# Kernel tuning notes

Hardware: AMD Instinct MI355X
Metric: run time of the kernel (lower is better)

Reference implementation:

```python
import jax, jax.numpy as jnp
import numpy as np

EPS = 1e-12
CHAMFER_W, NORM_W, EDGE_W = 1.0, 0.1, 0.5


def setup_inputs() -> dict:
    key = jax.random.key(0)
    ks = jax.random.split(key, 6)
    B, V, F, N = 8, 6890, 13776, 4096
    return {
        "predicted_vertices": jax.random.normal(ks[0], (B, V, 3), jnp.float32),
        "predicted_faces": jax.random.randint(ks[1], (F, 3), 0, V),
        "gt_vertices": jax.random.normal(ks[2], (B, V, 3), jnp.float32),
        "gt_faces": jax.random.randint(ks[3], (F, 3), 0, V),
        "rand_pred": jax.random.uniform(ks[4], (B, N, 3), jnp.float32),
        "rand_gt": jax.random.uniform(ks[5], (B, N, 3), jnp.float32),
    }


def _sample_points(vertices, faces, rnd):
    """Area-weighted surface sampling. vertices [B,V,3], faces [F,3], rnd [B,N,3].
    Returns (points [B,N,3], normals [B,N,3])."""
    tri = vertices[:, faces]                       # [B,F,3,3]
    v0, v1, v2 = tri[:, :, 0], tri[:, :, 1], tri[:, :, 2]
    cross = jnp.cross(v1 - v0, v2 - v0)            # [B,F,3]
    cn = jnp.linalg.norm(cross, axis=-1)           # [B,F]
    area = 0.5 * cn
    normals = cross / (cn[..., None] + EPS)
    cdf = jnp.cumsum(area, axis=1)
    cdf = cdf / (cdf[:, -1:] + EPS)
    u, r1, r2 = rnd[..., 0], rnd[..., 1], rnd[..., 2]
    idx = jax.vmap(jnp.searchsorted)(cdf, u)       # [B,N] inverse-CDF face pick
    idx = jnp.clip(idx, 0, faces.shape[0] - 1)
    g = lambda x: jnp.take_along_axis(x, idx[..., None], axis=1)
    p0, p1, p2 = g(v0), g(v1), g(v2)
    su = jnp.sqrt(r1)[..., None]                   # sqrt trick -> uniform barycentric
    w0 = 1.0 - su
    w1 = su * (1.0 - r2[..., None])
    w2 = su * r2[..., None]
    return w0 * p0 + w1 * p1 + w2 * p2, g(normals)


def reference(predicted_vertices, predicted_faces, gt_vertices, gt_faces, rand_pred, rand_gt):
    # NOTE: faithful to the source, which samples BOTH clouds from the predicted
    # mesh (copy-paste bug): gt cloud = second independent sample of pred mesh.
    pc, pn = _sample_points(predicted_vertices, predicted_faces, rand_pred)
    gc, gn = _sample_points(predicted_vertices, predicted_faces, rand_gt)

    # squared-distance chamfer: [B,N,N]
    d = (jnp.sum(pc * pc, -1)[:, :, None]
         + jnp.sum(gc * gc, -1)[:, None, :]
         - 2.0 * jnp.einsum('bnd,bmd->bnm', pc, gc))
    dist1 = jnp.min(d, axis=2)
    dist2 = jnp.min(d, axis=1)
    chamfer_loss = jnp.mean(dist1) + jnp.mean(dist2)

    # normal loss: cosine mismatch with nearest-neighbor normals
    nn = jnp.argmin(d, axis=2)                     # [B,N]
    gn_nn = jnp.take_along_axis(gn, nn[..., None], axis=1)
    norm_loss = jnp.mean(1.0 - jnp.abs(jnp.sum(pn * gn_nn, axis=-1)))

    # edge loss: mean squared edge length over the 3 edges of every face
    pv, pf = predicted_vertices, predicted_faces
    e01 = pv[:, pf[:, 0]] - pv[:, pf[:, 1]]
    e12 = pv[:, pf[:, 1]] - pv[:, pf[:, 2]]
    e20 = pv[:, pf[:, 2]] - pv[:, pf[:, 0]]
    edge_loss = (jnp.mean(jnp.sum(e01 * e01, -1))
                 + jnp.mean(jnp.sum(e12 * e12, -1))
                 + jnp.mean(jnp.sum(e20 * e20, -1))) / 3.0

    return CHAMFER_W * chamfer_loss + NORM_W * norm_loss + EDGE_W * edge_loss
```

## Files before the change

kernel.cpp:

```cpp
#include <hip/hip_runtime.h>

#define EPSF 1e-12f
#define FLTMAX 3.402823466e+38f

constexpr int B = 8, V = 6890, F = 13776, N = 4096;
constexpr int BF = B * F;
constexpr int BN = B * N;
constexpr int CHUNK = 512;
constexpr int NCHUNK = (F + CHUNK - 1) / CHUNK;

__device__ __forceinline__ unsigned enc_f(float f) {
  unsigned b = __float_as_uint(f);
  return (b & 0x80000000u) ? ~b : (b | 0x80000000u);
}
__device__ __forceinline__ float dec_f(unsigned u) {
  return (u & 0x80000000u) ? __uint_as_float(u & 0x7FFFFFFFu) : __uint_as_float(~u);
}

__device__ __forceinline__ float block_sum_256(float v, float* s4) {
  #pragma unroll
  for (int off = 32; off > 0; off >>= 1) v += __shfl_down(v, off, 64);
  __syncthreads();
  if ((threadIdx.x & 63) == 0) s4[threadIdx.x >> 6] = v;
  __syncthreads();
  return s4[0] + s4[1] + s4[2] + s4[3];
}

__global__ void init_kernel(unsigned long long* __restrict__ best1,
                            unsigned* __restrict__ best2, float* __restrict__ acc) {
  int i = blockIdx.x * 256 + threadIdx.x;
  best1[i] = ~0ull;
  best2[i] = ~0u;
  if (i < 4) acc[i] = 0.f;
}

__global__ void face_kernel(const float* __restrict__ pv, const int* __restrict__ pf,
                            float* __restrict__ area, float* __restrict__ nrm,
                            float* __restrict__ acc) {
  __shared__ float s4[4];
  int idx = blockIdx.x * 256 + threadIdx.x;
  float es = 0.f;
  if (idx < BF) {
    int b = idx / F, f = idx - b * F;
    int i0 = pf[f * 3 + 0], i1 = pf[f * 3 + 1], i2 = pf[f * 3 + 2];
    const float* vb = pv + (size_t)b * V * 3;
    float x0 = vb[i0 * 3 + 0], y0 = vb[i0 * 3 + 1], z0 = vb[i0 * 3 + 2];
    float x1 = vb[i1 * 3 + 0], y1 = vb[i1 * 3 + 1], z1 = vb[i1 * 3 + 2];
    float x2 = vb[i2 * 3 + 0], y2 = vb[i2 * 3 + 1], z2 = vb[i2 * 3 + 2];
    float ax = x1 - x0, ay = y1 - y0, az = z1 - z0;
    float bx = x2 - x0, by = y2 - y0, bz = z2 - z0;
    float cx = ay * bz - az * by;
    float cy = az * bx - ax * bz;
    float cz = ax * by - ay * bx;
    float cn = sqrtf(cx * cx + cy * cy + cz * cz);
    area[idx] = 0.5f * cn;
    float inv = 1.f / (cn + EPSF);
    nrm[(size_t)idx * 3 + 0] = cx * inv;
    nrm[(size_t)idx * 3 + 1] = cy * inv;
    nrm[(size_t)idx * 3 + 2] = cz * inv;
    float ex = x0 - x1, ey = y0 - y1, ez = z0 - z1;
    es = ex * ex + ey * ey + ez * ez;
    ex = x1 - x2; ey = y1 - y2; ez = z1 - z2;
    es += ex * ex + ey * ey + ez * ez;
    es += bx * bx + by * by + bz * bz;
  }
  float tot = block_sum_256(es, s4);
  if (threadIdx.x == 0) atomicAdd(&acc[3], tot);
}

__global__ void scan_chunks(float* __restrict__ cdf, float* __restrict__ csum) {
  int b = blockIdx.x / NCHUNK, ck = blockIdx.x % NCHUNK;
  float* c = cdf + (size_t)b * F;
  int lane = threadIdx.x & 63, wid = threadIdx.x >> 6;
  int i0 = ck * CHUNK + 2 * threadIdx.x, i1 = i0 + 1;
  float a0 = (i0 < F) ? c[i0] : 0.f;
  float a1 = (i1 < F) ? c[i1] : 0.f;
  float ts = a0 + a1;
  float x = ts;
  #pragma unroll
  for (int off = 1; off < 64; off <<= 1) {
    float y = __shfl_up(x, off, 64);
    if (lane >= off) x += y;
  }
  __shared__ float wsum[4];
  if (lane == 63) wsum[wid] = x;
  __syncthreads();
  float woff = 0.f;
  for (int w = 0; w < wid; ++w) woff += wsum[w];
  float excl = woff + x - ts;
  if (i0 < F) c[i0] = excl + a0;
  if (i1 < F) c[i1] = excl + ts;
  if (threadIdx.x == 255) csum[b * NCHUNK + ck] = woff + x;
}

__global__ void scan_sums(float* __restrict__ csum, float* __restrict__ totals) {
  int b = threadIdx.x;
  if (b < B) {
    float s = 0.f;
    for (int k = 0; k < NCHUNK; ++k) { s += csum[b * NCHUNK + k]; csum[b * NCHUNK + k] = s; }
    totals[b] = s;
  }
}

__global__ void sample_kernel(const float* __restrict__ pv, const int* __restrict__ pf,
                              const float* __restrict__ cdf, const float* __restrict__ csum,
                              const float* __restrict__ totals, const float* __restrict__ nrm,
                              const float* __restrict__ rp, const float* __restrict__ rg,
                              float* __restrict__ pc, float* __restrict__ pn,
                              float* __restrict__ gc, float* __restrict__ gn) {
  int idx = blockIdx.x * 256 + threadIdx.x;
  if (idx >= 2 * BN) return;
  int set = (idx >= BN) ? 1 : 0;
  int i = idx - set * BN;
  int b = i / N;
  const float* r = (set ? rg : rp) + (size_t)i * 3;
  float u = r[0], r1 = r[1], r2 = r[2];
  float target = u * (totals[b] + EPSF);
  const float* cs = csum + b * NCHUNK;
  int lo = 0, hi = NCHUNK;
  while (lo < hi) { int mid = (lo + hi) >> 1; if (cs[mid] < target) lo = mid + 1; else hi = mid; }
  int k = lo < NCHUNK ? lo : NCHUNK - 1;
  float off = (k > 0) ? cs[k - 1] : 0.f;
  float t2 = target - off;
  const float* c = cdf + (size_t)b * F;
  int base = k * CHUNK;
  int lo2 = 0, hi2 = CHUNK;
  while (lo2 < hi2) {
    int mid = (lo2 + hi2) >> 1;
    int gi = base + mid;
    float v = (gi < F) ? c[gi] : FLTMAX;
    if (v < t2) lo2 = mid + 1; else hi2 = mid;
  }
  int f = base + lo2;
  if (f > F - 1) f = F - 1;
  int i0 = pf[f * 3 + 0], i1 = pf[f * 3 + 1], i2 = pf[f * 3 + 2];
  const float* vb = pv + (size_t)b * V * 3;
  float su = sqrtf(r1);
  float w0 = 1.f - su, w1 = su * (1.f - r2), w2 = su * r2;
  float px = w0 * vb[i0 * 3 + 0] + w1 * vb[i1 * 3 + 0] + w2 * vb[i2 * 3 + 0];
  float py = w0 * vb[i0 * 3 + 1] + w1 * vb[i1 * 3 + 1] + w2 * vb[i2 * 3 + 1];
  float pz = w0 * vb[i0 * 3 + 2] + w1 * vb[i1 * 3 + 2] + w2 * vb[i2 * 3 + 2];
  float* pts = (set ? gc : pc) + (size_t)i * 3;
  float* pns = (set ? gn : pn) + (size_t)i * 3;
  pts[0] = px; pts[1] = py; pts[2] = pz;
  size_t nb = ((size_t)b * F + f) * 3;
  pns[0] = nrm[nb + 0]; pns[1] = nrm[nb + 1]; pns[2] = nrm[nb + 2];
}

__global__ __launch_bounds__(256, 4) void chamfer_kernel(
    const float* __restrict__ pc, const float* __restrict__ gc,
    unsigned long long* __restrict__ best1, unsigned* __restrict__ best2) {
  __shared__ float4 tile[256];
  bool is1 = blockIdx.x < 1024;
  int blk = is1 ? blockIdx.x : blockIdx.x - 1024;
  int b = blk >> 7;
  int nchunk = (blk >> 3) & 15, mchunk = blk & 7;
  int n = nchunk * 256 + threadIdx.x;
  int mbase = mchunk * 512;
  const float* own   = (is1 ? pc : gc) + ((size_t)b * N + n) * 3;
  const float* other = (is1 ? gc : pc) + (size_t)b * N * 3;
  float px = own[0], py = own[1], pz = own[2];
  float pp = px * px + py * py + pz * pz;
  float qx = -2.f * px, qy = -2.f * py, qz = -2.f * pz;
  float bd0 = FLTMAX, bd1 = FLTMAX, bd2 = FLTMAX, bd3 = FLTMAX;
  int bi0 = 0, bi1 = 0, bi2 = 0, bi3 = 0;
  for (int stage = 0; stage < 2; ++stage) {
    int mb = mbase + stage * 256;
    const float* g = other + (size_t)(mb + threadIdx.x) * 3;
    float gx = g[0], gy = g[1], gz = g[2];
    __syncthreads();
    tile[threadIdx.x] = make_float4(gx, gy, gz, gx * gx + gy * gy + gz * gz);
    __syncthreads();
    if (is1) {
      #pragma unroll 4
      for (int k = 0; k < 64; ++k) {
        int j = 4 * k;
        float4 t0 = tile[j], t1 = tile[j + 1], t2 = tile[j + 2], t3 = tile[j + 3];
        float d0 = fmaf(qx, t0.x, fmaf(qy, t0.y, fmaf(qz, t0.z, pp + t0.w)));
        float d1 = fmaf(qx, t1.x, fmaf(qy, t1.y, fmaf(qz, t1.z, pp + t1.w)));
        float d2 = fmaf(qx, t2.x, fmaf(qy, t2.y, fmaf(qz, t2.z, pp + t2.w)));
        float d3 = fmaf(qx, t3.x, fmaf(qy, t3.y, fmaf(qz, t3.z, pp + t3.w)));
        if (d0 < bd0) { bd0 = d0; bi0 = mb + j; }
        if (d1 < bd1) { bd1 = d1; bi1 = mb + j + 1; }
        if (d2 < bd2) { bd2 = d2; bi2 = mb + j + 2; }
        if (d3 < bd3) { bd3 = d3; bi3 = mb + j + 3; }
      }
    } else {
      #pragma unroll 4
      for (int k = 0; k < 64; ++k) {
        int j = 4 * k;
        float4 t0 = tile[j], t1 = tile[j + 1], t2 = tile[j + 2], t3 = tile[j + 3];
        float d0 = fmaf(qx, t0.x, fmaf(qy, t0.y, fmaf(qz, t0.z, pp + t0.w)));
        float d1 = fmaf(qx, t1.x, fmaf(qy, t1.y, fmaf(qz, t1.z, pp + t1.w)));
        float d2 = fmaf(qx, t2.x, fmaf(qy, t2.y, fmaf(qz, t2.z, pp + t2.w)));
        float d3 = fmaf(qx, t3.x, fmaf(qy, t3.y, fmaf(qz, t3.z, pp + t3.w)));
        bd0 = fminf(bd0, d0); bd1 = fminf(bd1, d1);
        bd2 = fminf(bd2, d2); bd3 = fminf(bd3, d3);
      }
    }
  }
  if (is1) {
    if (bd1 < bd0 || (bd1 == bd0 && bi1 < bi0)) { bd0 = bd1; bi0 = bi1; }
    if (bd3 < bd2 || (bd3 == bd2 && bi3 < bi2)) { bd2 = bd3; bi2 = bi3; }
    if (bd2 < bd0 || (bd2 == bd0 && bi2 < bi0)) { bd0 = bd2; bi0 = bi2; }
    unsigned long long key = ((unsigned long long)enc_f(bd0) << 32) | (unsigned)bi0;
    atomicMin(&best1[(size_t)b * N + n], key);
  } else {
    bd0 = fminf(fminf(bd0, bd1), fminf(bd2, bd3));
    atomicMin(&best2[(size_t)b * N + n], enc_f(bd0));
  }
}

__global__ void finalize_kernel(const unsigned long long* __restrict__ best1,
                                const unsigned* __restrict__ best2,
                                const float* __restrict__ pn, const float* __restrict__ gn,
                                float* __restrict__ acc) {
  __shared__ float s4[4];
  int i = blockIdx.x * 256 + threadIdx.x;
  int b = i >> 12;
  unsigned long long k1 = best1[i];
  float d1 = dec_f((unsigned)(k1 >> 32));
  int m = (int)(unsigned)(k1 & 0xFFFFFFFFull);
  float d2 = dec_f(best2[i]);
  const float* a  = pn + (size_t)i * 3;
  const float* bb = gn + ((size_t)b * N + m) * 3;
  float nl = 1.f - fabsf(a[0] * bb[0] + a[1] * bb[1] + a[2] * bb[2]);
  float sd1 = block_sum_256(d1, s4);
  float sd2 = block_sum_256(d2, s4);
  float snl = block_sum_256(nl, s4);
  if (threadIdx.x == 0) {
    atomicAdd(&acc[0], sd1);
    atomicAdd(&acc[1], sd2);
    atomicAdd(&acc[2], snl);
  }
}

__global__ void final_kernel(const float* __restrict__ acc, float* __restrict__ out) {
  if (threadIdx.x == 0 && blockIdx.x == 0) {
    float inv_bn = 1.f / (float)BN;
    float chamfer = (acc[0] + acc[1]) * inv_bn;
    float nrm_l = acc[2] * inv_bn;
    float edge = acc[3] / (3.f * (float)BF);
    out[0] = 1.0f * chamfer + 0.1f * nrm_l + 0.5f * edge;
  }
}

extern "C" void kernel_launch(void* const* d_in, const int* in_sizes, int n_in,
                              void* d_out, int out_size, void* d_ws, size_t ws_size,
                              hipStream_t stream) {
  const float* pv = (const float*)d_in[0];
  const int*   pf = (const int*)d_in[1];
  const float* rp = (const float*)d_in[4];
  const float* rg = (const float*)d_in[5];
  float* out = (float*)d_out;

  unsigned long long* best1 = (unsigned long long*)d_ws;
  unsigned* best2 = (unsigned*)(best1 + BN);
  float* fws    = (float*)(best2 + BN);
  float* cdf    = fws;
  float* nrm    = cdf + BF;
  float* pc     = nrm + (size_t)BF * 3;
  float* pn     = pc + (size_t)BN * 3;
  float* gc     = pn + (size_t)BN * 3;
  float* gn     = gc + (size_t)BN * 3;
  float* csum   = gn + (size_t)BN * 3;
  float* totals = csum + B * NCHUNK;
  float* acc    = totals + B;

  init_kernel<<<BN / 256, 256, 0, stream>>>(best1, best2, acc);
  face_kernel<<<(BF + 255) / 256, 256, 0, stream>>>(pv, pf, cdf, nrm, acc);
  scan_chunks<<<B * NCHUNK, 256, 0, stream>>>(cdf, csum);
  scan_sums<<<1, 64, 0, stream>>>(csum, totals);
  sample_kernel<<<(2 * BN) / 256, 256, 0, stream>>>(pv, pf, cdf, csum, totals, nrm,
                                                    rp, rg, pc, pn, gc, gn);
  chamfer_kernel<<<2048, 256, 0, stream>>>(pc, gc, best1, best2);
  finalize_kernel<<<BN / 256, 256, 0, stream>>>(best1, best2, pn, gn, acc);
  final_kernel<<<1, 64, 0, stream>>>(acc, out);
}
```

Before: 131.2 us.

## Fuse face, scan, and init kernels; use float4 layouts and last-block finalize

Fuses initialization, face geometry, edge-length partial sums and the per-chunk CDF scan into one kernel. The sampler now finds the chunk with a linear walk over chunk sums instead of a separate scan-sums pass. Points and normals are stored as float4, with the squared norm precomputed in the w slot. The chamfer kernel reads candidate points straight from global memory instead of a shared tile and raises the occupancy hint. A ticket counter lets the last finalize block write the output, which removes the final kernel. Together these cut the launch count from eight to four, at the cost of relying on cache behaviour for the untiled chamfer loads and on atomic-ticket ordering being correct.

New measurement: 125.5 us. 1.05x faster.

```diff
diff --git a/kernel.cpp b/kernel.cpp
--- a/kernel.cpp
+++ b/kernel.cpp
@@ -8,6 +8,7 @@
 constexpr int BN = B * N;
 constexpr int CHUNK = 512;
 constexpr int NCHUNK = (F + CHUNK - 1) / CHUNK;
+constexpr int SCAN_BLOCKS = B * NCHUNK;
 
 __device__ __forceinline__ unsigned enc_f(float f) {
   unsigned b = __float_as_uint(f);
@@ -26,55 +27,53 @@
   return s4[0] + s4[1] + s4[2] + s4[3];
 }
 
-__global__ void init_kernel(unsigned long long* __restrict__ best1,
-                            unsigned* __restrict__ best2, float* __restrict__ acc) {
-  int i = blockIdx.x * 256 + threadIdx.x;
-  best1[i] = ~0ull;
-  best2[i] = ~0u;
-  if (i < 4) acc[i] = 0.f;
-}
-
-__global__ void face_kernel(const float* __restrict__ pv, const int* __restrict__ pf,
-                            float* __restrict__ area, float* __restrict__ nrm,
-                            float* __restrict__ acc) {
+__device__ __forceinline__ float face_geom(const float* __restrict__ pv,
+                                           const int* __restrict__ pf,
+                                           int b, int f, float4* __restrict__ nrm4,
+                                           float& es) {
+  if (f >= F) return 0.f;
+  int i0 = pf[f * 3 + 0], i1 = pf[f * 3 + 1], i2 = pf[f * 3 + 2];
+  const float* vb = pv + (size_t)b * V * 3;
+  float x0 = vb[i0 * 3 + 0], y0 = vb[i0 * 3 + 1], z0 = vb[i0 * 3 + 2];
+  float x1 = vb[i1 * 3 + 0], y1 = vb[i1 * 3 + 1], z1 = vb[i1 * 3 + 2];
+  float x2 = vb[i2 * 3 + 0], y2 = vb[i2 * 3 + 1], z2 = vb[i2 * 3 + 2];
+  float ax = x1 - x0, ay = y1 - y0, az = z1 - z0;
+  float bx = x2 - x0, by = y2 - y0, bz = z2 - z0;
+  float cx = ay * bz - az * by;
+  float cy = az * bx - ax * bz;
+  float cz = ax * by - ay * bx;
+  float cn = sqrtf(cx * cx + cy * cy + cz * cz);
+  float inv = 1.f / (cn + EPSF);
+  nrm4[(size_t)b * F + f] = make_float4(cx * inv, cy * inv, cz * inv, 0.f);
+  float ex = x0 - x1, ey = y0 - y1, ez = z0 - z1;
+  es += ex * ex + ey * ey + ez * ez;
+  ex = x1 - x2; ey = y1 - y2; ez = z1 - z2;
+  es += ex * ex + ey * ey + ez * ez;
+  es += bx * bx + by * by + bz * bz;
+  return 0.5f * cn;
+}
+
+__global__ __launch_bounds__(256) void scan_faces_kernel(
+    const float* __restrict__ pv, const int* __restrict__ pf,
+    float* __restrict__ cdf, float* __restrict__ csum, float4* __restrict__ nrm4,
+    float* __restrict__ edgep,
+    unsigned long long* __restrict__ best1, unsigned* __restrict__ best2,
+    float* __restrict__ acc, unsigned* __restrict__ cnt) {
+  __shared__ float wsum[4];
   __shared__ float s4[4];
-  int idx = blockIdx.x * 256 + threadIdx.x;
+  int b = blockIdx.x / NCHUNK, ck = blockIdx.x % NCHUNK;
+  int lane = threadIdx.x & 63, wid = threadIdx.x >> 6;
+
+  int gid = blockIdx.x * 256 + threadIdx.x;
+  if (gid < BN) { best1[gid] = ~0ull; best2[gid] = ~0u; }
+  if (gid < 2) acc[gid] = 0.f;
+  if (gid == 2) *cnt = 0u;
+
+  int f0 = ck * CHUNK + 2 * threadIdx.x;
   float es = 0.f;
-  if (idx < BF) {
-    int b = idx / F, f = idx - b * F;
-    int i0 = pf[f * 3 + 0], i1 = pf[f * 3 + 1], i2 = pf[f * 3 + 2];
-    const float* vb = pv + (size_t)b * V * 3;
-    float x0 = vb[i0 * 3 + 0], y0 = vb[i0 * 3 + 1], z0 = vb[i0 * 3 + 2];
-    float x1 = vb[i1 * 3 + 0], y1 = vb[i1 * 3 + 1], z1 = vb[i1 * 3 + 2];
-    float x2 = vb[i2 * 3 + 0], y2 = vb[i2 * 3 + 1], z2 = vb[i2 * 3 + 2];
-    float ax = x1 - x0, ay = y1 - y0, az = z1 - z0;
-    float bx = x2 - x0, by = y2 - y0, bz = z2 - z0;
-    float cx = ay * bz - az * by;
-    float cy = az * bx - ax * bz;
-    float cz = ax * by - ay * bx;
-    float cn = sqrtf(cx * cx + cy * cy + cz * cz);
-    area[idx] = 0.5f * cn;
-    float inv = 1.f / (cn + EPSF);
-    nrm[(size_t)idx * 3 + 0] = cx * inv;
-    nrm[(size_t)idx * 3 + 1] = cy * inv;
-    nrm[(size_t)idx * 3 + 2] = cz * inv;
-    float ex = x0 - x1, ey = y0 - y1, ez = z0 - z1;
-    es = ex * ex + ey * ey + ez * ez;
-    ex = x1 - x2; ey = y1 - y2; ez = z1 - z2;
-    es += ex * ex + ey * ey + ez * ez;
-    es += bx * bx + by * by + bz * bz;
-  }
-  float tot = block_sum_256(es, s4);
-  if (threadIdx.x == 0) atomicAdd(&acc[3], tot);
-}
-
-__global__ void scan_chunks(float* __restrict__ cdf, float* __restrict__ csum) {
-  int b = blockIdx.x / NCHUNK, ck = blockIdx.x % NCHUNK;
-  float* c = cdf + (size_t)b * F;
-  int lane = threadIdx.x & 63, wid = threadIdx.x >> 6;
-  int i0 = ck * CHUNK + 2 * threadIdx.x, i1 = i0 + 1;
-  float a0 = (i0 < F) ? c[i0] : 0.f;
-  float a1 = (i1 < F) ? c[i1] : 0.f;
+  float a0 = face_geom(pv, pf, b, f0, nrm4, es);
+  float a1 = face_geom(pv, pf, b, f0 + 1, nrm4, es);
+
   float ts = a0 + a1;
   float x = ts;
   #pragma unroll
@@ -82,32 +81,27 @@
     float y = __shfl_up(x, off, 64);
     if (lane >= off) x += y;
   }
-  __shared__ float wsum[4];
   if (lane == 63) wsum[wid] = x;
   __syncthreads();
   float woff = 0.f;
   for (int w = 0; w < wid; ++w) woff += wsum[w];
   float excl = woff + x - ts;
-  if (i0 < F) c[i0] = excl + a0;
-  if (i1 < F) c[i1] = excl + ts;
-  if (threadIdx.x == 255) csum[b * NCHUNK + ck] = woff + x;
-}
-
-__global__ void scan_sums(float* __restrict__ csum, float* __restrict__ totals) {
-  int b = threadIdx.x;
-  if (b < B) {
-    float s = 0.f;
-    for (int k = 0; k < NCHUNK; ++k) { s += csum[b * NCHUNK + k]; csum[b * NCHUNK + k] = s; }
-    totals[b] = s;
-  }
-}
-
-__global__ void sample_kernel(const float* __restrict__ pv, const int* __restrict__ pf,
-                              const float* __restrict__ cdf, const float* __restrict__ csum,
-                              const float* __restrict__ totals, const float* __restrict__ nrm,
-                              const float* __restrict__ rp, const float* __restrict__ rg,
-                              float* __restrict__ pc, float* __restrict__ pn,
-                              float* __restrict__ gc, float* __restrict__ gn) {
+  size_t g0 = (size_t)b * F + f0;
+  if (f0 < F) cdf[g0] = excl + a0;
+  if (f0 + 1 < F) cdf[g0 + 1] = excl + ts;
+  if (threadIdx.x == 255) csum[blockIdx.x] = woff + x;
+
+  float te = block_sum_256(es, s4);
+  if (threadIdx.x == 0) edgep[blockIdx.x] = te;
+}
+
+__global__ __launch_bounds__(256) void sample_kernel(
+    const float* __restrict__ pv, const int* __restrict__ pf,
+    const float* __restrict__ cdf, const float* __restrict__ csum,
+    const float4* __restrict__ nrm4,
+    const float* __restrict__ rp, const float* __restrict__ rg,
+    float4* __restrict__ pc4, float4* __restrict__ pn4,
+    float4* __restrict__ gc4, float4* __restrict__ gn4) {
   int idx = blockIdx.x * 256 + threadIdx.x;
   if (idx >= 2 * BN) return;
   int set = (idx >= BN) ? 1 : 0;
@@ -115,24 +109,30 @@
   int b = i / N;
   const float* r = (set ? rg : rp) + (size_t)i * 3;
   float u = r[0], r1 = r[1], r2 = r[2];
-  float target = u * (totals[b] + EPSF);
+
   const float* cs = csum + b * NCHUNK;
-  int lo = 0, hi = NCHUNK;
-  while (lo < hi) { int mid = (lo + hi) >> 1; if (cs[mid] < target) lo = mid + 1; else hi = mid; }
-  int k = lo < NCHUNK ? lo : NCHUNK - 1;
-  float off = (k > 0) ? cs[k - 1] : 0.f;
-  float t2 = target - off;
-  const float* c = cdf + (size_t)b * F;
+  float total = 0.f;
+  #pragma unroll
+  for (int k2 = 0; k2 < NCHUNK; ++k2) total += cs[k2];
+  float target = u * (total + EPSF);
+
+  int k = 0;
+  float s = cs[0];
+  while (s < target && k < NCHUNK - 1) { ++k; s += cs[k]; }
+  float prefix = s - cs[k];
+  float t2 = target - prefix;
+
+  const float* c = cdf + (size_t)b * F + k * CHUNK;
   int base = k * CHUNK;
-  int lo2 = 0, hi2 = CHUNK;
-  while (lo2 < hi2) {
-    int mid = (lo2 + hi2) >> 1;
-    int gi = base + mid;
-    float v = (gi < F) ? c[gi] : FLTMAX;
-    if (v < t2) lo2 = mid + 1; else hi2 = mid;
-  }
-  int f = base + lo2;
+  int lo = 0, hi = CHUNK;
+  while (lo < hi) {
+    int mid = (lo + hi) >> 1;
+    float v = (base + mid < F) ? c[mid] : FLTMAX;
+    if (v < t2) lo = mid + 1; else hi = mid;
+  }
+  int f = base + lo;
   if (f > F - 1) f = F - 1;
+
   int i0 = pf[f * 3 + 0], i1 = pf[f * 3 + 1], i2 = pf[f * 3 + 2];
   const float* vb = pv + (size_t)b * V * 3;
   float su = sqrtf(r1);
@@ -140,108 +140,96 @@
   float px = w0 * vb[i0 * 3 + 0] + w1 * vb[i1 * 3 + 0] + w2 * vb[i2 * 3 + 0];
   float py = w0 * vb[i0 * 3 + 1] + w1 * vb[i1 * 3 + 1] + w2 * vb[i2 * 3 + 1];
   float pz = w0 * vb[i0 * 3 + 2] + w1 * vb[i1 * 3 + 2] + w2 * vb[i2 * 3 + 2];
-  float* pts = (set ? gc : pc) + (size_t)i * 3;
-  float* pns = (set ? gn : pn) + (size_t)i * 3;
-  pts[0] = px; pts[1] = py; pts[2] = pz;
-  size_t nb = ((size_t)b * F + f) * 3;
-  pns[0] = nrm[nb + 0]; pns[1] = nrm[nb + 1]; pns[2] = nrm[nb + 2];
-}
-
-__global__ __launch_bounds__(256, 4) void chamfer_kernel(
-    const float* __restrict__ pc, const float* __restrict__ gc,
+  float4* pts = (set ? gc4 : pc4);
+  float4* pns = (set ? gn4 : pn4);
+  pts[i] = make_float4(px, py, pz, px * px + py * py + pz * pz);
+  pns[i] = nrm4[(size_t)b * F + f];
+}
+
+__global__ __launch_bounds__(256, 8) void chamfer_kernel(
+    const float4* __restrict__ pc4, const float4* __restrict__ gc4,
     unsigned long long* __restrict__ best1, unsigned* __restrict__ best2) {
-  __shared__ float4 tile[256];
-  bool is1 = blockIdx.x < 1024;
-  int blk = is1 ? blockIdx.x : blockIdx.x - 1024;
-  int b = blk >> 7;
-  int nchunk = (blk >> 3) & 15, mchunk = blk & 7;
-  int n = nchunk * 256 + threadIdx.x;
-  int mbase = mchunk * 512;
-  const float* own   = (is1 ? pc : gc) + ((size_t)b * N + n) * 3;
-  const float* other = (is1 ? gc : pc) + (size_t)b * N * 3;
-  float px = own[0], py = own[1], pz = own[2];
-  float pp = px * px + py * py + pz * pz;
-  float qx = -2.f * px, qy = -2.f * py, qz = -2.f * pz;
-  float bd0 = FLTMAX, bd1 = FLTMAX, bd2 = FLTMAX, bd3 = FLTMAX;
-  int bi0 = 0, bi1 = 0, bi2 = 0, bi3 = 0;
-  for (int stage = 0; stage < 2; ++stage) {
-    int mb = mbase + stage * 256;
-    const float* g = other + (size_t)(mb + threadIdx.x) * 3;
-    float gx = g[0], gy = g[1], gz = g[2];
-    __syncthreads();
-    tile[threadIdx.x] = make_float4(gx, gy, gz, gx * gx + gy * gy + gz * gz);
-    __syncthreads();
-    if (is1) {
-      #pragma unroll 4
-      for (int k = 0; k < 64; ++k) {
-        int j = 4 * k;
-        float4 t0 = tile[j], t1 = tile[j + 1], t2 = tile[j + 2], t3 = tile[j + 3];
-        float d0 = fmaf(qx, t0.x, fmaf(qy, t0.y, fmaf(qz, t0.z, pp + t0.w)));
-        float d1 = fmaf(qx, t1.x, fmaf(qy, t1.y, fmaf(qz, t1.z, pp + t1.w)));
-        float d2 = fmaf(qx, t2.x, fmaf(qy, t2.y, fmaf(qz, t2.z, pp + t2.w)));
-        float d3 = fmaf(qx, t3.x, fmaf(qy, t3.y, fmaf(qz, t3.z, pp + t3.w)));
-        if (d0 < bd0) { bd0 = d0; bi0 = mb + j; }
-        if (d1 < bd1) { bd1 = d1; bi1 = mb + j + 1; }
-        if (d2 < bd2) { bd2 = d2; bi2 = mb + j + 2; }
-        if (d3 < bd3) { bd3 = d3; bi3 = mb + j + 3; }
-      }
-    } else {
-      #pragma unroll 4
-      for (int k = 0; k < 64; ++k) {
-        int j = 4 * k;
-        float4 t0 = tile[j], t1 = tile[j + 1], t2 = tile[j + 2], t3 = tile[j + 3];
-        float d0 = fmaf(qx, t0.x, fmaf(qy, t0.y, fmaf(qz, t0.z, pp + t0.w)));
-        float d1 = fmaf(qx, t1.x, fmaf(qy, t1.y, fmaf(qz, t1.z, pp + t1.w)));
-        float d2 = fmaf(qx, t2.x, fmaf(qy, t2.y, fmaf(qz, t2.z, pp + t2.w)));
-        float d3 = fmaf(qx, t3.x, fmaf(qy, t3.y, fmaf(qz, t3.z, pp + t3.w)));
-        bd0 = fminf(bd0, d0); bd1 = fminf(bd1, d1);
-        bd2 = fminf(bd2, d2); bd3 = fminf(bd3, d3);
-      }
+  const bool is1 = blockIdx.x < 1024;
+  const int blk = is1 ? blockIdx.x : blockIdx.x - 1024;
+  const int b = blk >> 7;
+  const int nchunk = (blk >> 3) & 15, mchunk = blk & 7;
+  const int n = nchunk * 256 + threadIdx.x;
+  const int mbase = mchunk * 512;
+  const float4 p = (is1 ? pc4 : gc4)[(size_t)b * N + n];
+  const float4* __restrict__ other = (is1 ? gc4 : pc4) + (size_t)b * N + mbase;
+  const float qx = -2.f * p.x, qy = -2.f * p.y, qz = -2.f * p.z;
+  const float pp = p.w;
+
+  if (is1) {
+    float bd0 = FLTMAX, bd1 = FLTMAX, bd2 = FLTMAX, bd3 = FLTMAX;
+    int bi0 = 0, bi1 = 0, bi2 = 0, bi3 = 0;
+    #pragma unroll 2
+    for (int j = 0; j < 512; j += 4) {
+      float4 t0 = other[j], t1 = other[j + 1], t2 = other[j + 2], t3 = other[j + 3];
+      float d0 = fmaf(qx, t0.x, fmaf(qy, t0.y, fmaf(qz, t0.z, pp + t0.w)));
+      float d1 = fmaf(qx, t1.x, fmaf(qy, t1.y, fmaf(qz, t1.z, pp + t1.w)));
+      float d2 = fmaf(qx, t2.x, fmaf(qy, t2.y, fmaf(qz, t2.z, pp + t2.w)));
+      float d3 = fmaf(qx, t3.x, fmaf(qy, t3.y, fmaf(qz, t3.z, pp + t3.w)));
+      if (d0 < bd0) { bd0 = d0; bi0 = mbase + j; }
+      if (d1 < bd1) { bd1 = d1; bi1 = mbase + j + 1; }
+      if (d2 < bd2) { bd2 = d2; bi2 = mbase + j + 2; }
+      if (d3 < bd3) { bd3 = d3; bi3 = mbase + j + 3; }
     }
-  }
-  if (is1) {
     if (bd1 < bd0 || (bd1 == bd0 && bi1 < bi0)) { bd0 = bd1; bi0 = bi1; }
     if (bd3 < bd2 || (bd3 == bd2 && bi3 < bi2)) { bd2 = bd3; bi2 = bi3; }
     if (bd2 < bd0 || (bd2 == bd0 && bi2 < bi0)) { bd0 = bd2; bi0 = bi2; }
     unsigned long long key = ((unsigned long long)enc_f(bd0) << 32) | (unsigned)bi0;
     atomicMin(&best1[(size_t)b * N + n], key);
   } else {
-    bd0 = fminf(fminf(bd0, bd1), fminf(bd2, bd3));
-    atomicMin(&best2[(size_t)b * N + n], enc_f(bd0));
-  }
-}
-
-__global__ void finalize_kernel(const unsigned long long* __restrict__ best1,
-                                const unsigned* __restrict__ best2,
-                                const float* __restrict__ pn, const float* __restrict__ gn,
-                                float* __restrict__ acc) {
+    float bda = FLTMAX, bdb = FLTMAX;
+    #pragma unroll 2
+    for (int j = 0; j < 512; j += 4) {
+      float4 t0 = other[j], t1 = other[j + 1], t2 = other[j + 2], t3 = other[j + 3];
+      float d0 = fmaf(qx, t0.x, fmaf(qy, t0.y, fmaf(qz, t0.z, pp + t0.w)));
+      float d1 = fmaf(qx, t1.x, fmaf(qy, t1.y, fmaf(qz, t1.z, pp + t1.w)));
+      float d2 = fmaf(qx, t2.x, fmaf(qy, t2.y, fmaf(qz, t2.z, pp + t2.w)));
+      float d3 = fmaf(qx, t3.x, fmaf(qy, t3.y, fmaf(qz, t3.z, pp + t3.w)));
+      bda = fminf(fminf(d0, d1), bda);
+      bdb = fminf(fminf(d2, d3), bdb);
+    }
+    atomicMin(&best2[(size_t)b * N + n], enc_f(fminf(bda, bdb)));
+  }
+}
+
+__global__ __launch_bounds__(256) void finalize_kernel(
+    const unsigned long long* __restrict__ best1, const unsigned* __restrict__ best2,
+    const float4* __restrict__ pn4, const float4* __restrict__ gn4,
+    const float* __restrict__ edgep,
+    float* __restrict__ acc, unsigned* __restrict__ cnt, float* __restrict__ out) {
   __shared__ float s4[4];
+  __shared__ unsigned ticket;
   int i = blockIdx.x * 256 + threadIdx.x;
   int b = i >> 12;
   unsigned long long k1 = best1[i];
   float d1 = dec_f((unsigned)(k1 >> 32));
   int m = (int)(unsigned)(k1 & 0xFFFFFFFFull);
   float d2 = dec_f(best2[i]);
-  const float* a  = pn + (size_t)i * 3;
-  const float* bb = gn + ((size_t)b * N + m) * 3;
-  float nl = 1.f - fabsf(a[0] * bb[0] + a[1] * bb[1] + a[2] * bb[2]);
-  float sd1 = block_sum_256(d1, s4);
-  float sd2 = block_sum_256(d2, s4);
-  float snl = block_sum_256(nl, s4);
+  float4 a = pn4[i];
+  float4 g = gn4[((size_t)b << 12) + m];
+  float nl = 1.f - fabsf(a.x * g.x + a.y * g.y + a.z * g.z);
+  float sd = block_sum_256(d1 + d2, s4);
+  float sn = block_sum_256(nl, s4);
   if (threadIdx.x == 0) {
-    atomicAdd(&acc[0], sd1);
-    atomicAdd(&acc[1], sd2);
-    atomicAdd(&acc[2], snl);
-  }
-}
-
-__global__ void final_kernel(const float* __restrict__ acc, float* __restrict__ out) {
-  if (threadIdx.x == 0 && blockIdx.x == 0) {
-    float inv_bn = 1.f / (float)BN;
-    float chamfer = (acc[0] + acc[1]) * inv_bn;
-    float nrm_l = acc[2] * inv_bn;
-    float edge = acc[3] / (3.f * (float)BF);
-    out[0] = 1.0f * chamfer + 0.1f * nrm_l + 0.5f * edge;
+    atomicAdd(&acc[0], sd);
+    atomicAdd(&acc[1], sn);
+    __threadfence();
+    ticket = atomicAdd(cnt, 1u);
+  }
+  __syncthreads();
+  if (ticket == 127) {
+    float e = (threadIdx.x < SCAN_BLOCKS) ? edgep[threadIdx.x] : 0.f;
+    float te = block_sum_256(e, s4);
+    if (threadIdx.x == 0) {
+      float chamf = atomicAdd(&acc[0], 0.f);
+      float nsum  = atomicAdd(&acc[1], 0.f);
+      float inv_bn = 1.f / (float)BN;
+      out[0] = chamf * inv_bn + 0.1f * (nsum * inv_bn) + 0.5f * (te / (3.f * (float)BF));
+    }
   }
 }
 
@@ -256,24 +244,22 @@
 
   unsigned long long* best1 = (unsigned long long*)d_ws;
   unsigned* best2 = (unsigned*)(best1 + BN);
-  float* fws    = (float*)(best2 + BN);
-  float* cdf    = fws;
-  float* nrm    = cdf + BF;
-  float* pc     = nrm + (size_t)BF * 3;
-  float* pn     = pc + (size_t)BN * 3;
-  float* gc     = pn + (size_t)BN * 3;
-  float* gn     = gc + (size_t)BN * 3;
-  float* csum   = gn + (size_t)BN * 3;
-  float* totals = csum + B * NCHUNK;
-  float* acc    = totals + B;
-
-  init_kernel<<<BN / 256, 256, 0, stream>>>(best1, best2, acc);
-  face_kernel<<<(BF + 255) / 256, 256, 0, stream>>>(pv, pf, cdf, nrm, acc);
-  scan_chunks<<<B * NCHUNK, 256, 0, stream>>>(cdf, csum);
-  scan_sums<<<1, 64, 0, stream>>>(csum, totals);
-  sample_kernel<<<(2 * BN) / 256, 256, 0, stream>>>(pv, pf, cdf, csum, totals, nrm,
-                                                    rp, rg, pc, pn, gc, gn);
-  chamfer_kernel<<<2048, 256, 0, stream>>>(pc, gc, best1, best2);
-  finalize_kernel<<<BN / 256, 256, 0, stream>>>(best1, best2, pn, gn, acc);
-  final_kernel<<<1, 64, 0, stream>>>(acc, out);
-}
+  float4* pc4  = (float4*)(best2 + BN);
+  float4* pn4  = pc4 + BN;
+  float4* gc4  = pn4 + BN;
+  float4* gn4  = gc4 + BN;
+  float4* nrm4 = gn4 + BN;
+  float* cdf   = (float*)(nrm4 + BF);
+  float* csum  = cdf + BF;
+  float* edgep = csum + SCAN_BLOCKS;
+  float* acc   = edgep + SCAN_BLOCKS;
+  unsigned* cnt = (unsigned*)(acc + 2);
+
+  scan_faces_kernel<<<SCAN_BLOCKS, 256, 0, stream>>>(pv, pf, cdf, csum, nrm4, edgep,
+                                                     best1, best2, acc, cnt);
+  sample_kernel<<<(2 * BN) / 256, 256, 0, stream>>>(pv, pf, cdf, csum, nrm4,
+                                                    rp, rg, pc4, pn4, gc4, gn4);
+  chamfer_kernel<<<2048, 256, 0, stream>>>(pc4, gc4, best1, best2);
+  finalize_kernel<<<BN / 256, 256, 0, stream>>>(best1, best2, pn4, gn4, edgep,
+                                                acc, cnt, out);
+}
```
